# Optimization experiments

Hardware: AMD Instinct MI355X
Metric: run time of the kernel (lower is better)

## Reference

```python
import jax, jax.numpy as jnp
import numpy as np

D_MODEL = 1024
NHEAD = 16
D_K = D_MODEL // NHEAD
D_FF = 4096
EPS = 1e-5


def _layer_norm(x, g, b):
    mu = jnp.mean(x, axis=-1, keepdims=True)
    var = jnp.mean(jnp.square(x - mu), axis=-1, keepdims=True)
    return (x - mu) * jax.lax.rsqrt(var + EPS) * g + b


def setup_inputs() -> dict:
    key = jax.random.key(0)
    ks = jax.random.split(key, 14)
    s = 0.02
    d = {
        'src': jax.random.normal(ks[0], (4, 2048, D_MODEL), dtype=jnp.float32),
        'Wq': jax.random.normal(ks[1], (D_MODEL, D_MODEL), dtype=jnp.float32) * s,
        'bq': jnp.zeros((D_MODEL,), jnp.float32),
        'Wk': jax.random.normal(ks[2], (D_MODEL, D_MODEL), dtype=jnp.float32) * s,
        'bk': jnp.zeros((D_MODEL,), jnp.float32),
        'Wv': jax.random.normal(ks[3], (D_MODEL, D_MODEL), dtype=jnp.float32) * s,
        'bv': jnp.zeros((D_MODEL,), jnp.float32),
        'Wo': jax.random.normal(ks[4], (D_MODEL, D_MODEL), dtype=jnp.float32) * s,
        'bo': jnp.zeros((D_MODEL,), jnp.float32),
        'W1': jax.random.normal(ks[5], (D_MODEL, D_FF), dtype=jnp.float32) * s,
        'b1': jnp.zeros((D_FF,), jnp.float32),
        'W2': jax.random.normal(ks[6], (D_FF, D_MODEL), dtype=jnp.float32) * s,
        'b2': jnp.zeros((D_MODEL,), jnp.float32),
        'ln1_g': jnp.ones((D_MODEL,), jnp.float32),
        'ln1_b': jnp.zeros((D_MODEL,), jnp.float32),
        'ln2_g': jnp.ones((D_MODEL,), jnp.float32),
        'ln2_b': jnp.zeros((D_MODEL,), jnp.float32),
    }
    return d


def reference(src, Wq, bq, Wk, bk, Wv, bv, Wo, bo, W1, b1, W2, b2,
              ln1_g, ln1_b, ln2_g, ln2_b):
    B, L, _ = src.shape
    # QKV projections -> [B, H, L, d_k]
    def heads(x, W, b):
        y = x @ W + b
        return y.reshape(B, L, NHEAD, D_K).transpose(0, 2, 1, 3)
    Q = heads(src, Wq, bq)
    K = heads(src, Wk, bk)
    V = heads(src, Wv, bv)
    # scores [B, H, Lq, Lk]
    scores = jnp.einsum('bhqd,bhkd->bhqk', Q, K) / jnp.sqrt(jnp.float32(D_K))
    attn = jax.nn.softmax(scores, axis=-1)
    ctx = jnp.einsum('bhqk,bhkd->bhqd', attn, V)
    ctx = ctx.transpose(0, 2, 1, 3).reshape(B, L, D_MODEL)
    attn_out = ctx @ Wo + bo
    x = _layer_norm(src + attn_out, ln1_g, ln1_b)
    ff = jax.nn.relu(x @ W1 + b1) @ W2 + b2
    return _layer_norm(x + ff, ln2_g, ln2_b)
```

## Files before the change

### kernel.cpp

```cpp
#include <hip/hip_runtime.h>
#include <hip/hip_bf16.h>


#define D_MODEL 1024
#define SEQ     2048
#define BATCH   4
#define NHEAD   16
#define D_FF    4096
#define M_ROWS  (BATCH * SEQ)

typedef __attribute__((ext_vector_type(8))) short bf16x8;
typedef __attribute__((ext_vector_type(4))) float f32x4;

__device__ __forceinline__ ushort f2bf(float x) {
    unsigned u = __float_as_uint(x);
    unsigned r = (u + 0x7FFFu + ((u >> 16) & 1u)) >> 16;
    return (ushort)r;
}

__global__ __launch_bounds__(256) void cast_kernel(
    const float* __restrict__ x, ushort* __restrict__ y)
{
    const size_t i = ((size_t)blockIdx.x * 256 + threadIdx.x) * 4;
    float4 v = *(const float4*)&x[i];
    ushort4 o;
    o.x = f2bf(v.x); o.y = f2bf(v.y); o.z = f2bf(v.z); o.w = f2bf(v.w);
    *(ushort4*)&y[i] = o;
}

__global__ __launch_bounds__(256) void transpose_cast_kernel(
    const float* __restrict__ W, ushort* __restrict__ Wt, int R, int C)
{
    __shared__ float tile[64][68];
    const int c0 = blockIdx.x * 64, r0 = blockIdx.y * 64;
    const int t  = threadIdx.x;
    const int tc  = (t & 15) * 4;
    const int tr4 = (t >> 4) * 4;
#pragma unroll
    for (int i = 0; i < 4; ++i) {
        float4 v = *(const float4*)&W[(size_t)(r0 + tr4 + i) * C + c0 + tc];
        *(float4*)&tile[tr4 + i][tc] = v;
    }
    __syncthreads();
#pragma unroll
    for (int i = 0; i < 4; ++i) {
        const int nn = tr4 + i;
        ushort4 o;
        o.x = f2bf(tile[tc + 0][nn]);
        o.y = f2bf(tile[tc + 1][nn]);
        o.z = f2bf(tile[tc + 2][nn]);
        o.w = f2bf(tile[tc + 3][nn]);
        *(ushort4*)&Wt[(size_t)(c0 + nn) * R + r0 + tc] = o;
    }
}

template <int MODE>
__global__ __launch_bounds__(256) void gemm_mfma(
    const ushort* __restrict__ A, const ushort* __restrict__ Bt,
    const float* __restrict__ bias, void* __restrict__ C,
    int M, int N, int K, float scale)
{
    __shared__ __attribute__((aligned(16))) ushort As[128 * 32];
    __shared__ __attribute__((aligned(16))) ushort Bs[128 * 32];

    const int t    = threadIdx.x;
    const int lane = t & 63;
    const int wave = t >> 6;
    const int bm   = blockIdx.y * 128;
    const int bn   = blockIdx.x * 128;
    const int wm   = (wave & 1) * 64;
    const int wn   = (wave >> 1) * 64;

    const int fr = lane & 15;
    const int fk = (lane >> 4) * 8;

    f32x4 acc[4][4];
#pragma unroll
    for (int i = 0; i < 4; ++i)
#pragma unroll
        for (int j = 0; j < 4; ++j)
            acc[i][j] = (f32x4){0.f, 0.f, 0.f, 0.f};

    for (int k0 = 0; k0 < K; k0 += 32) {
#pragma unroll
        for (int r = 0; r < 2; ++r) {
            const int c   = r * 256 + t;
            const int row = c >> 2;
            const int kc  = (c & 3) * 8;
            __builtin_amdgcn_global_load_lds(
                (const __attribute__((address_space(1))) void*)(A + (size_t)(bm + row) * K + k0 + kc),
                (__attribute__((address_space(3))) void*)(As + c * 8), 16, 0, 0);
            __builtin_amdgcn_global_load_lds(
                (const __attribute__((address_space(1))) void*)(Bt + (size_t)(bn + row) * K + k0 + kc),
                (__attribute__((address_space(3))) void*)(Bs + c * 8), 16, 0, 0);
        }
        __syncthreads();

        bf16x8 af[4], bfr[4];
#pragma unroll
        for (int i = 0; i < 4; ++i)
            af[i] = *(const bf16x8*)&As[(wm + i * 16 + fr) * 32 + fk];
#pragma unroll
        for (int j = 0; j < 4; ++j)
            bfr[j] = *(const bf16x8*)&Bs[(wn + j * 16 + fr) * 32 + fk];

#pragma unroll
        for (int i = 0; i < 4; ++i)
#pragma unroll
            for (int j = 0; j < 4; ++j)
                acc[i][j] = __builtin_amdgcn_mfma_f32_16x16x32_bf16(af[i], bfr[j], acc[i][j], 0, 0, 0);
        __syncthreads();
    }

    const int rbase = (lane >> 4) * 4;
    float bcol[4];
#pragma unroll
    for (int j = 0; j < 4; ++j) bcol[j] = bias[bn + wn + j * 16 + fr];

#pragma unroll
    for (int i = 0; i < 4; ++i) {
#pragma unroll
        for (int j = 0; j < 4; ++j) {
            const int col  = bn + wn + j * 16 + fr;
            const int row0 = bm + wm + i * 16 + rbase;
            float v[4];
#pragma unroll
            for (int r = 0; r < 4; ++r) v[r] = acc[i][j][r] + bcol[j];

            if (MODE == 0) {
#pragma unroll
                for (int r = 0; r < 4; ++r)
                    ((float*)C)[(size_t)(row0 + r) * N + col] = v[r];
            } else if (MODE == 2) {
#pragma unroll
                for (int r = 0; r < 4; ++r)
                    ((ushort*)C)[(size_t)(row0 + r) * N + col] = f2bf(fmaxf(v[r], 0.f));
            } else if (MODE == 1) {
                const int h = col >> 6, d = col & 63;
#pragma unroll
                for (int r = 0; r < 4; ++r) {
                    const int row = row0 + r;
                    const int b = row >> 11, l = row & 2047;
                    ((ushort*)C)[(((size_t)(b * NHEAD + h) * SEQ + l) << 6) + d] = f2bf(v[r] * scale);
                }
            } else {
                const int b = row0 >> 11, l0 = row0 & 2047;
                const int h = col >> 6,  d = col & 63;
                ushort4 o;
                o.x = f2bf(v[0]); o.y = f2bf(v[1]); o.z = f2bf(v[2]); o.w = f2bf(v[3]);
                *(ushort4*)&((ushort*)C)[(((size_t)(b * NHEAD + h) * 64 + d) << 11) + l0] = o;
            }
        }
    }
}

__global__ __launch_bounds__(256, 3) void attn_mfma(
    const ushort* __restrict__ Q, const ushort* __restrict__ K,
    const ushort* __restrict__ Vt, ushort* __restrict__ CTX)
{
    __shared__ __attribute__((aligned(16))) ushort Ks[64 * 64];
    __shared__ __attribute__((aligned(16))) ushort Vs[64 * 64];
    __shared__ __attribute__((aligned(16))) ushort Ps[128 * 64];

    const int t    = threadIdx.x;
    const int lane = t & 63;
    const int w    = t >> 6;
    const int l15  = lane & 15;
    const int quad = lane >> 4;
    const int bh   = blockIdx.y;
    const int q0   = blockIdx.x * 128;

    bf16x8 afq[2][2];
    const ushort* Qbase = Q + ((size_t)bh * SEQ + q0 + w * 32) * 64;
#pragma unroll
    for (int i = 0; i < 2; ++i)
#pragma unroll
        for (int ks = 0; ks < 2; ++ks)
            afq[i][ks] = *(const bf16x8*)&Qbase[(i * 16 + l15) * 64 + quad * 8 + ks * 32];

    f32x4 oacc[2][4];
#pragma unroll
    for (int i = 0; i < 2; ++i)
#pragma unroll
        for (int d = 0; d < 4; ++d) oacc[i][d] = (f32x4){0.f, 0.f, 0.f, 0.f};
    float lrun[2][4];
#pragma unroll
    for (int i = 0; i < 2; ++i)
#pragma unroll
        for (int r = 0; r < 4; ++r) lrun[i][r] = 0.f;

    const ushort* Kb  = K  + ((size_t)bh * SEQ) * 64;
    const ushort* Vtb = Vt + ((size_t)bh * 64) * SEQ;

    const int srow0 = t >> 3;
    const int sc8   = t & 7;

    for (int kk0 = 0; kk0 < SEQ; kk0 += 64) {
        bf16x8 kv0 = *(const bf16x8*)&Kb[(size_t)(kk0 + srow0) * 64 + sc8 * 8];
        bf16x8 kv1 = *(const bf16x8*)&Kb[(size_t)(kk0 + srow0 + 32) * 64 + sc8 * 8];
        bf16x8 vv0 = *(const bf16x8*)&Vtb[(size_t)srow0 * SEQ + kk0 + sc8 * 8];
        bf16x8 vv1 = *(const bf16x8*)&Vtb[(size_t)(srow0 + 32) * SEQ + kk0 + sc8 * 8];

        __syncthreads();

        {
            const int pr0 = (srow0 & 3) * 16 + (srow0 >> 2);
            const int pr1 = ((srow0 + 32) & 3) * 16 + ((srow0 + 32) >> 2);
            *(bf16x8*)&Ks[pr0 * 64 + ((sc8 ^ (pr0 & 7)) << 3)] = kv0;
            *(bf16x8*)&Ks[pr1 * 64 + ((sc8 ^ (pr1 & 7)) << 3)] = kv1;
            *(bf16x8*)&Vs[srow0 * 64 + ((sc8 ^ (srow0 & 7)) << 3)] = vv0;
            *(bf16x8*)&Vs[(srow0 + 32) * 64 + ((sc8 ^ ((srow0 + 32) & 7)) << 3)] = vv1;
        }
        __syncthreads();

        f32x4 sacc[2][4];
#pragma unroll
        for (int i = 0; i < 2; ++i)
#pragma unroll
            for (int j = 0; j < 4; ++j) sacc[i][j] = (f32x4){0.f, 0.f, 0.f, 0.f};
        const int swz0 = (quad ^ (l15 & 7)) << 3;
        const int swz1 = ((quad + 4) ^ (l15 & 7)) << 3;
#pragma unroll
        for (int j = 0; j < 4; ++j) {
            const int krow = (j * 16 + l15) * 64;
            bf16x8 bk0 = *(const bf16x8*)&Ks[krow + swz0];
            bf16x8 bk1 = *(const bf16x8*)&Ks[krow + swz1];
            sacc[0][j] = __builtin_amdgcn_mfma_f32_16x16x32_bf16(afq[0][0], bk0, sacc[0][j], 0, 0, 0);
            sacc[0][j] = __builtin_amdgcn_mfma_f32_16x16x32_bf16(afq[0][1], bk1, sacc[0][j], 0, 0, 0);
            sacc[1][j] = __builtin_amdgcn_mfma_f32_16x16x32_bf16(afq[1][0], bk0, sacc[1][j], 0, 0, 0);
            sacc[1][j] = __builtin_amdgcn_mfma_f32_16x16x32_bf16(afq[1][1], bk1, sacc[1][j], 0, 0, 0);
        }

#pragma unroll
        for (int i = 0; i < 2; ++i) {
#pragma unroll
            for (int r = 0; r < 4; ++r) {
                const float p0 = __expf(sacc[i][0][r]);
                const float p1 = __expf(sacc[i][1][r]);
                const float p2 = __expf(sacc[i][2][r]);
                const float p3 = __expf(sacc[i][3][r]);
                lrun[i][r] += (p0 + p1) + (p2 + p3);
                const unsigned u0 = __builtin_amdgcn_perm(
                    __float_as_uint(p1), __float_as_uint(p0), 0x07060302u);
                const unsigned u1 = __builtin_amdgcn_perm(
                    __float_as_uint(p3), __float_as_uint(p2), 0x07060302u);
                const int prow = w * 32 + i * 16 + quad * 4 + r;
                const int off = prow * 64 + (((l15 >> 1) ^ (prow & 7)) << 3) + (l15 & 1) * 4;
                *(unsigned long long*)&Ps[off] =
                    (unsigned long long)u0 | ((unsigned long long)u1 << 32);
            }
        }

        bf16x8 ap[2][2];
#pragma unroll
        for (int i = 0; i < 2; ++i) {
            const int prow = (w * 32 + i * 16 + l15) * 64;
            ap[i][0] = *(const bf16x8*)&Ps[prow + swz0];
            ap[i][1] = *(const bf16x8*)&Ps[prow + swz1];
        }
#pragma unroll
        for (int dt = 0; dt < 4; ++dt) {
            const int vrow = (dt * 16 + l15) * 64;
            bf16x8 bv0 = *(const bf16x8*)&Vs[vrow + swz0];
            bf16x8 bv1 = *(const bf16x8*)&Vs[vrow + swz1];
            oacc[0][dt] = __builtin_amdgcn_mfma_f32_16x16x32_bf16(ap[0][0], bv0, oacc[0][dt], 0, 0, 0);
            oacc[0][dt] = __builtin_amdgcn_mfma_f32_16x16x32_bf16(ap[0][1], bv1, oacc[0][dt], 0, 0, 0);
            oacc[1][dt] = __builtin_amdgcn_mfma_f32_16x16x32_bf16(ap[1][0], bv0, oacc[1][dt], 0, 0, 0);
            oacc[1][dt] = __builtin_amdgcn_mfma_f32_16x16x32_bf16(ap[1][1], bv1, oacc[1][dt], 0, 0, 0);
        }
    }

    const int b = bh >> 4, h = bh & 15;
#pragma unroll
    for (int i = 0; i < 2; ++i) {
#pragma unroll
        for (int r = 0; r < 4; ++r) {
            float l = lrun[i][r];
#pragma unroll
            for (int m = 1; m < 16; m <<= 1) l += __shfl_xor(l, m, 64);
            const float inv = 1.f / l;
            const int tok = q0 + w * 32 + i * 16 + quad * 4 + r;
            ushort* op = CTX + ((size_t)(b * SEQ + tok)) * D_MODEL + h * 64;
#pragma unroll
            for (int dt = 0; dt < 4; ++dt)
                op[dt * 16 + l15] = f2bf(oacc[i][dt][r] * inv);
        }
    }
}

template <bool WRITE_BF>
__global__ __launch_bounds__(256) void ln_kernel(
    const float* __restrict__ y, const float* __restrict__ res,
    const float* __restrict__ g, const float* __restrict__ bta,
    float* __restrict__ out, ushort* __restrict__ out_bf)
{
    __shared__ float red[4];
    const int t = threadIdx.x;
    const size_t base = (size_t)blockIdx.x * D_MODEL + t * 4;

    float4 a = *(const float4*)&y[base];
    float4 r = *(const float4*)&res[base];
    const float v0 = a.x + r.x, v1 = a.y + r.y, v2 = a.z + r.z, v3 = a.w + r.w;

    float s = v0 + v1 + v2 + v3;
#pragma unroll
    for (int o = 32; o > 0; o >>= 1) s += __shfl_down(s, o, 64);
    if ((t & 63) == 0) red[t >> 6] = s;
    __syncthreads();
    const float mu = (red[0] + red[1] + red[2] + red[3]) * (1.f / 1024.f);

    const float d0 = v0 - mu, d1 = v1 - mu, d2 = v2 - mu, d3 = v3 - mu;
    float sq = d0 * d0 + d1 * d1 + d2 * d2 + d3 * d3;
#pragma unroll
    for (int o = 32; o > 0; o >>= 1) sq += __shfl_down(sq, o, 64);
    __syncthreads();
    if ((t & 63) == 0) red[t >> 6] = sq;
    __syncthreads();
    const float var  = (red[0] + red[1] + red[2] + red[3]) * (1.f / 1024.f);
    const float rstd = rsqrtf(var + 1e-5f);

    const int c = t * 4;
    float4 gv = *(const float4*)&g[c];
    float4 bv = *(const float4*)&bta[c];
    float4 o4;
    o4.x = d0 * rstd * gv.x + bv.x;
    o4.y = d1 * rstd * gv.y + bv.y;
    o4.z = d2 * rstd * gv.z + bv.z;
    o4.w = d3 * rstd * gv.w + bv.w;
    *(float4*)&out[base] = o4;
    if (WRITE_BF) {
        ushort4 ob;
        ob.x = f2bf(o4.x); ob.y = f2bf(o4.y); ob.z = f2bf(o4.z); ob.w = f2bf(o4.w);
        *(ushort4*)&out_bf[base] = ob;
    }
}

extern "C" void kernel_launch(void* const* d_in, const int* in_sizes, int n_in,
                              void* d_out, int out_size, void* d_ws, size_t ws_size,
                              hipStream_t stream)
{
    const float* src = (const float*)d_in[0];
    const float* Wq  = (const float*)d_in[1];  const float* bq = (const float*)d_in[2];
    const float* Wk  = (const float*)d_in[3];  const float* bk = (const float*)d_in[4];
    const float* Wv  = (const float*)d_in[5];  const float* bv = (const float*)d_in[6];
    const float* Wo  = (const float*)d_in[7];  const float* bo = (const float*)d_in[8];
    const float* W1  = (const float*)d_in[9];  const float* b1 = (const float*)d_in[10];
    const float* W2  = (const float*)d_in[11]; const float* b2 = (const float*)d_in[12];
    const float* g1  = (const float*)d_in[13]; const float* be1 = (const float*)d_in[14];
    const float* g2  = (const float*)d_in[15]; const float* be2 = (const float*)d_in[16];
    float* out = (float*)d_out;

    char* ws = (char*)d_ws;
    const size_t MB = 1024 * 1024;
    ushort* Qb   = (ushort*)(ws);
    ushort* Kb   = (ushort*)(ws + 16 * MB);
    ushort* Vtb  = (ushort*)(ws + 32 * MB);
    ushort* CTXb = (ushort*)(ws + 48 * MB);
    ushort* FFb  = (ushort*)(ws);
    float*  Xf   = (float*) (ws + 64 * MB);
    ushort* X1b  = (ushort*)(ws + 96 * MB);
    ushort* SRCb = (ushort*)(ws + 112 * MB);
    ushort* W1t  = (ushort*)(ws + 112 * MB);
    ushort* W2t  = (ushort*)(ws + 120 * MB);
    ushort* Wqt  = (ushort*)(ws + 128 * MB);
    ushort* Wkt  = (ushort*)(ws + 130 * MB);
    ushort* Wvt  = (ushort*)(ws + 132 * MB);
    ushort* Wot  = (ushort*)(ws + 134 * MB);

    dim3 blk(256);

    cast_kernel<<<dim3(M_ROWS * D_MODEL / 1024), blk, 0, stream>>>(src, SRCb);
    transpose_cast_kernel<<<dim3(16, 16), blk, 0, stream>>>(Wq, Wqt, D_MODEL, D_MODEL);
    transpose_cast_kernel<<<dim3(16, 16), blk, 0, stream>>>(Wk, Wkt, D_MODEL, D_MODEL);
    transpose_cast_kernel<<<dim3(16, 16), blk, 0, stream>>>(Wv, Wvt, D_MODEL, D_MODEL);
    transpose_cast_kernel<<<dim3(16, 16), blk, 0, stream>>>(Wo, Wot, D_MODEL, D_MODEL);

    gemm_mfma<1><<<dim3(8, 64), blk, 0, stream>>>(SRCb, Wqt, bq, Qb, M_ROWS, D_MODEL, D_MODEL, 0.125f);
    gemm_mfma<1><<<dim3(8, 64), blk, 0, stream>>>(SRCb, Wkt, bk, Kb, M_ROWS, D_MODEL, D_MODEL, 1.0f);
    gemm_mfma<3><<<dim3(8, 64), blk, 0, stream>>>(SRCb, Wvt, bv, Vtb, M_ROWS, D_MODEL, D_MODEL, 1.0f);

    transpose_cast_kernel<<<dim3(64, 16), blk, 0, stream>>>(W1, W1t, D_MODEL, D_FF);
    transpose_cast_kernel<<<dim3(16, 64), blk, 0, stream>>>(W2, W2t, D_FF, D_MODEL);

    attn_mfma<<<dim3(SEQ / 128, BATCH * NHEAD), blk, 0, stream>>>(Qb, Kb, Vtb, CTXb);

    gemm_mfma<0><<<dim3(8, 64), blk, 0, stream>>>(CTXb, Wot, bo, Xf, M_ROWS, D_MODEL, D_MODEL, 1.0f);

    ln_kernel<true><<<M_ROWS, blk, 0, stream>>>(Xf, src, g1, be1, Xf, X1b);

    gemm_mfma<2><<<dim3(32, 64), blk, 0, stream>>>(X1b, W1t, b1, FFb, M_ROWS, D_FF, D_MODEL, 1.0f);

    gemm_mfma<0><<<dim3(8, 64), blk, 0, stream>>>(FFb, W2t, b2, out, M_ROWS, D_MODEL, D_FF, 1.0f);

    ln_kernel<false><<<M_ROWS, blk, 0, stream>>>(out, Xf, g2, be2, out, nullptr);
}
```

Baseline: 601.7 us.

## Swizzle GEMM LDS layout and remap block IDs for XCD-aware L2 locality

Applies an XOR swizzle to the 16-byte chunks written into LDS by global_load_lds, so the MFMA fragment reads from As/Bs avoid bank conflicts. It also remaps the linear block ID so that consecutive blocks, which are assigned to the 8 XCDs round-robin, land on contiguous tiles per XCD. This is meant to improve L2 reuse in both the GEMMs and the attention kernel. The remap assumes grid dimensions divisible by 8 and a power-of-two x-dimension passed as nxshift.

```diff
diff --git a/kernel.cpp b/kernel.cpp
--- a/kernel.cpp
+++ b/kernel.cpp
@@ -16,6 +16,10 @@
     unsigned u = __float_as_uint(x);
     unsigned r = (u + 0x7FFFu + ((u >> 16) & 1u)) >> 16;
     return (ushort)r;
+}
+
+__device__ __forceinline__ int swz_off(int r, int q) {
+    return ((r >> 1) << 6) | (((((r & 1) << 2) | q) ^ ((r >> 1) & 7)) << 3);
 }
 
 __global__ __launch_bounds__(256) void cast_kernel(
@@ -58,7 +62,7 @@
 __global__ __launch_bounds__(256) void gemm_mfma(
     const ushort* __restrict__ A, const ushort* __restrict__ Bt,
     const float* __restrict__ bias, void* __restrict__ C,
-    int M, int N, int K, float scale)
+    int M, int N, int K, float scale, int nxshift)
 {
     __shared__ __attribute__((aligned(16))) ushort As[128 * 32];
     __shared__ __attribute__((aligned(16))) ushort Bs[128 * 32];
@@ -66,13 +70,18 @@
     const int t    = threadIdx.x;
     const int lane = t & 63;
     const int wave = t >> 6;
-    const int bm   = blockIdx.y * 128;
-    const int bn   = blockIdx.x * 128;
+
+    const int bid   = blockIdx.y * gridDim.x + blockIdx.x;
+    const int idx   = bid >> 3;
+    const int bxs   = idx & ((1 << nxshift) - 1);
+    const int bys   = (bid & 7) * (gridDim.y >> 3) + (idx >> nxshift);
+    const int bm    = bys * 128;
+    const int bn    = bxs * 128;
+
     const int wm   = (wave & 1) * 64;
     const int wn   = (wave >> 1) * 64;
-
-    const int fr = lane & 15;
-    const int fk = (lane >> 4) * 8;
+    const int fr   = lane & 15;
+    const int quad = lane >> 4;
 
     f32x4 acc[4][4];
 #pragma unroll
@@ -84,25 +93,26 @@
     for (int k0 = 0; k0 < K; k0 += 32) {
 #pragma unroll
         for (int r = 0; r < 2; ++r) {
-            const int c   = r * 256 + t;
+            const int s   = r * 256 + t;
+            const int c   = (s & ~7) | ((s & 7) ^ ((s >> 3) & 7));
             const int row = c >> 2;
             const int kc  = (c & 3) * 8;
             __builtin_amdgcn_global_load_lds(
                 (const __attribute__((address_space(1))) void*)(A + (size_t)(bm + row) * K + k0 + kc),
-                (__attribute__((address_space(3))) void*)(As + c * 8), 16, 0, 0);
+                (__attribute__((address_space(3))) void*)(As + s * 8), 16, 0, 0);
             __builtin_amdgcn_global_load_lds(
                 (const __attribute__((address_space(1))) void*)(Bt + (size_t)(bn + row) * K + k0 + kc),
-                (__attribute__((address_space(3))) void*)(Bs + c * 8), 16, 0, 0);
+                (__attribute__((address_space(3))) void*)(Bs + s * 8), 16, 0, 0);
         }
         __syncthreads();
 
         bf16x8 af[4], bfr[4];
 #pragma unroll
         for (int i = 0; i < 4; ++i)
-            af[i] = *(const bf16x8*)&As[(wm + i * 16 + fr) * 32 + fk];
+            af[i] = *(const bf16x8*)&As[swz_off(wm + i * 16 + fr, quad)];
 #pragma unroll
         for (int j = 0; j < 4; ++j)
-            bfr[j] = *(const bf16x8*)&Bs[(wn + j * 16 + fr) * 32 + fk];
+            bfr[j] = *(const bf16x8*)&Bs[swz_off(wn + j * 16 + fr, quad)];
 
 #pragma unroll
         for (int i = 0; i < 4; ++i)
@@ -112,7 +122,7 @@
         __syncthreads();
     }
 
-    const int rbase = (lane >> 4) * 4;
+    const int rbase = quad * 4;
     float bcol[4];
 #pragma unroll
     for (int j = 0; j < 4; ++j) bcol[j] = bias[bn + wn + j * 16 + fr];
@@ -167,8 +177,11 @@
     const int w    = t >> 6;
     const int l15  = lane & 15;
     const int quad = lane >> 4;
-    const int bh   = blockIdx.y;
-    const int q0   = blockIdx.x * 128;
+
+    const int bid = blockIdx.y * gridDim.x + blockIdx.x;
+    const int idx = bid >> 3;
+    const int bh  = (bid & 7) * 8 + (idx >> 4);
+    const int q0  = (idx & 15) * 128;
 
     bf16x8 afq[2][2];
     const ushort* Qbase = Q + ((size_t)bh * SEQ + q0 + w * 32) * 64;
@@ -375,22 +388,22 @@
     transpose_cast_kernel<<<dim3(16, 16), blk, 0, stream>>>(Wv, Wvt, D_MODEL, D_MODEL);
     transpose_cast_kernel<<<dim3(16, 16), blk, 0, stream>>>(Wo, Wot, D_MODEL, D_MODEL);
 
-    gemm_mfma<1><<<dim3(8, 64), blk, 0, stream>>>(SRCb, Wqt, bq, Qb, M_ROWS, D_MODEL, D_MODEL, 0.125f);
-    gemm_mfma<1><<<dim3(8, 64), blk, 0, stream>>>(SRCb, Wkt, bk, Kb, M_ROWS, D_MODEL, D_MODEL, 1.0f);
-    gemm_mfma<3><<<dim3(8, 64), blk, 0, stream>>>(SRCb, Wvt, bv, Vtb, M_ROWS, D_MODEL, D_MODEL, 1.0f);
+    gemm_mfma<1><<<dim3(8, 64), blk, 0, stream>>>(SRCb, Wqt, bq, Qb, M_ROWS, D_MODEL, D_MODEL, 0.125f, 3);
+    gemm_mfma<1><<<dim3(8, 64), blk, 0, stream>>>(SRCb, Wkt, bk, Kb, M_ROWS, D_MODEL, D_MODEL, 1.0f, 3);
+    gemm_mfma<3><<<dim3(8, 64), blk, 0, stream>>>(SRCb, Wvt, bv, Vtb, M_ROWS, D_MODEL, D_MODEL, 1.0f, 3);
 
     transpose_cast_kernel<<<dim3(64, 16), blk, 0, stream>>>(W1, W1t, D_MODEL, D_FF);
     transpose_cast_kernel<<<dim3(16, 64), blk, 0, stream>>>(W2, W2t, D_FF, D_MODEL);
 
     attn_mfma<<<dim3(SEQ / 128, BATCH * NHEAD), blk, 0, stream>>>(Qb, Kb, Vtb, CTXb);
 
-    gemm_mfma<0><<<dim3(8, 64), blk, 0, stream>>>(CTXb, Wot, bo, Xf, M_ROWS, D_MODEL, D_MODEL, 1.0f);
+    gemm_mfma<0><<<dim3(8, 64), blk, 0, stream>>>(CTXb, Wot, bo, Xf, M_ROWS, D_MODEL, D_MODEL, 1.0f, 3);
 
     ln_kernel<true><<<M_ROWS, blk, 0, stream>>>(Xf, src, g1, be1, Xf, X1b);
 
-    gemm_mfma<2><<<dim3(32, 64), blk, 0, stream>>>(X1b, W1t, b1, FFb, M_ROWS, D_FF, D_MODEL, 1.0f);
-
-    gemm_mfma<0><<<dim3(8, 64), blk, 0, stream>>>(FFb, W2t, b2, out, M_ROWS, D_MODEL, D_FF, 1.0f);
+    gemm_mfma<2><<<dim3(32, 64), blk, 0, stream>>>(X1b, W1t, b1, FFb, M_ROWS, D_FF, D_MODEL, 1.0f, 5);
+
+    gemm_mfma<0><<<dim3(8, 64), blk, 0, stream>>>(FFb, W2t, b2, out, M_ROWS, D_MODEL, D_FF, 1.0f, 3);
 
     ln_kernel<false><<<M_ROWS, blk, 0, stream>>>(out, Xf, g2, be2, out, nullptr);
 }
```

Result: faster. 570.8 us (-5.1%).
